# Optimization experiments

Hardware: AMD Instinct MI355X
Metric: run time of the kernel (lower is better)

Reference implementation:

```python
import jax, jax.numpy as jnp
import numpy as np

VOCAB = 45
MAX_LEN = 250
E = 1024
H = 8
F = 4096
L = 6
B = 32
S = 256


def layer_norm(x, g, b, eps=1e-5):
    m = x.mean(-1, keepdims=True)
    v = ((x - m) ** 2).mean(-1, keepdims=True)
    return (x - m) / jnp.sqrt(v + eps) * g + b


def setup_inputs() -> dict:
    key = jax.random.key(0)
    ks = jax.random.split(key, 20)
    s = 0.02
    inp = {
        "sequences": jax.random.randint(ks[0], (B, S), 1, VOCAB),  # avoid PAD id 0
        "token_emb": jax.random.normal(ks[1], (VOCAB, E), jnp.float32) * s,
        "dist_emb": jax.random.normal(ks[2], (MAX_LEN + 1, H), jnp.float32) * s,
        "Wqkv": jax.random.normal(ks[3], (L, 3 * E, E), jnp.float32) * s,
        "bqkv": jnp.zeros((L, 3 * E), jnp.float32),
        "Wo": jax.random.normal(ks[4], (L, E, E), jnp.float32) * s,
        "bo": jnp.zeros((L, E), jnp.float32),
        "W1": jax.random.normal(ks[5], (L, F, E), jnp.float32) * s,
        "b1": jnp.zeros((L, F), jnp.float32),
        "W2": jax.random.normal(ks[6], (L, E, F), jnp.float32) * s,
        "b2": jnp.zeros((L, E), jnp.float32),
        "ln1_g": jnp.ones((L, E), jnp.float32),
        "ln1_b": jnp.zeros((L, E), jnp.float32),
        "ln2_g": jnp.ones((L, E), jnp.float32),
        "ln2_b": jnp.zeros((L, E), jnp.float32),
        "fn_g": jnp.ones((E,), jnp.float32),
        "fn_b": jnp.zeros((E,), jnp.float32),
        "gen_W": jax.random.normal(ks[7], (VOCAB, E), jnp.float32) * s,
        "gen_b": jnp.zeros((VOCAB,), jnp.float32),
    }
    return inp


def reference(sequences, token_emb, dist_emb, Wqkv, bqkv, Wo, bo, W1, b1, W2, b2,
              ln1_g, ln1_b, ln2_g, ln2_b, fn_g, fn_b, gen_W, gen_b):
    Bsz, Slen = sequences.shape
    Emb = token_emb.shape[1]
    nH = dist_emb.shape[1]
    Dh = Emb // nH

    x = token_emb[sequences] * jnp.sqrt(jnp.float32(Emb))  # [B,S,E]

    idx = jnp.arange(Slen)
    dist = jnp.minimum(jnp.abs(idx[None, :] - idx[:, None]), dist_emb.shape[0] - 1)
    bias = jnp.transpose(dist_emb[dist], (2, 0, 1))  # [H,S,S]
    causal = idx[None, :] <= idx[:, None]  # key <= query (lower-triangular allowed)
    mask = jnp.where(causal[None, :, :], bias, jnp.float32(-1e9))  # [H,S,S]

    scale = 1.0 / jnp.sqrt(jnp.float32(Dh))
    nL = Wqkv.shape[0]
    for l in range(nL):
        qkv = x @ Wqkv[l].T + bqkv[l]  # [B,S,3E]
        q, k, v = jnp.split(qkv, 3, axis=-1)
        q = q.reshape(Bsz, Slen, nH, Dh)
        k = k.reshape(Bsz, Slen, nH, Dh)
        v = v.reshape(Bsz, Slen, nH, Dh)
        scores = jnp.einsum('bqhd,bkhd->bhqk', q, k) * scale + mask[None]
        attn = jax.nn.softmax(scores, axis=-1)
        o = jnp.einsum('bhqk,bkhd->bqhd', attn, v).reshape(Bsz, Slen, Emb)
        o = o @ Wo[l].T + bo[l]
        x = layer_norm(x + o, ln1_g[l], ln1_b[l])
        h = jax.nn.gelu(x @ W1[l].T + b1[l], approximate=False)
        h = h @ W2[l].T + b2[l]
        x = layer_norm(x + h, ln2_g[l], ln2_b[l])

    x = layer_norm(x, fn_g, fn_b)
    logits = x @ gen_W.T + gen_b  # [B,S,VOCAB]
    return logits
```

## Files before the change

kernel.cpp:

```cpp
#include <hip/hip_runtime.h>
#include <hip/hip_bf16.h>

typedef __hip_bfloat16 bf16;
typedef __attribute__((ext_vector_type(8))) short short8;
typedef __attribute__((ext_vector_type(4))) float f32x4;

#define GLB_AS(p) ((const __attribute__((address_space(1))) void*)(p))
#define LDS_AS(p) ((__attribute__((address_space(3))) void*)(p))

template<int EPI>
__global__ __launch_bounds__(512, 2) void gemm8p(
    const bf16* __restrict__ A, const bf16* __restrict__ Bm, bf16* __restrict__ C,
    int K, int lda, int ldb, int ldc, const float* __restrict__ bias)
{
    __shared__ __align__(16) bf16 Als[2][2][8192];
    __shared__ __align__(16) bf16 Bls[2][2][8192];

    const int tid  = threadIdx.x;
    const int wave = tid >> 6;
    const int lane = tid & 63;
    const int wr = wave >> 2;
    const int wc = wave & 3;

    const int Mt = gridDim.x, Nt = gridDim.y;
    int pid = blockIdx.y * Mt + blockIdx.x;
    const int cpx = (Mt * Nt) >> 3;
    pid = (pid & 7) * cpx + (pid >> 3);
    int m_t, n_t;
    {
        const int grpsz = 8 * Nt;
        const int grp = pid / grpsz;
        const int first = grp * 8;
        int rem = Mt - first; if (rem > 8) rem = 8;
        const int loc = pid - grp * grpsz;
        m_t = first + loc % rem;
        n_t = loc / rem;
    }
    const int m0 = m_t << 8;
    const int n0 = n_t << 8;
    const int nt = K >> 6;

    const int s_r  = tid >> 2;
    const int s_sl = ((tid & 3) ^ ((tid >> 3) & 3)) << 3;
    const bf16* As0 = A  + (long)(m0 + s_r) * lda + s_sl;
    const bf16* Bs0 = Bm + (long)(n0 + s_r) * ldb + s_sl;
    const long ldal = (long)lda << 7;
    const long ldbl = (long)ldb << 7;
    char* AB = (char*)Als;
    char* BB = (char*)Bls;
    const int wofs = wave << 10;

#define STAGE_A(d, kh, tt) do { \
    const bf16* g_ = As0 + ((long)(tt) << 6) + ((kh) << 5); \
    char* dst_ = AB + ((((d) << 1) + (kh)) << 14) + wofs; \
    __builtin_amdgcn_global_load_lds(GLB_AS(g_), LDS_AS(dst_), 16, 0, 0); \
    __builtin_amdgcn_global_load_lds(GLB_AS(g_ + ldal), LDS_AS(dst_ + 8192), 16, 0, 0); \
  } while (0)
#define STAGE_B(d, kh, tt) do { \
    const bf16* g_ = Bs0 + ((long)(tt) << 6) + ((kh) << 5); \
    char* dst_ = BB + ((((d) << 1) + (kh)) << 14) + wofs; \
    __builtin_amdgcn_global_load_lds(GLB_AS(g_), LDS_AS(dst_), 16, 0, 0); \
    __builtin_amdgcn_global_load_lds(GLB_AS(g_ + ldbl), LDS_AS(dst_ + 8192), 16, 0, 0); \
  } while (0)
#define BAR() do { asm volatile("" ::: "memory"); \
    __builtin_amdgcn_s_barrier(); asm volatile("" ::: "memory"); } while (0)

    STAGE_B(0, 0, 0); STAGE_A(0, 0, 0); STAGE_B(0, 1, 0); STAGE_A(0, 1, 0);
    STAGE_B(1, 0, 1); STAGE_A(1, 0, 1); STAGE_B(1, 1, 1);

    f32x4 acc[8][4];
#pragma unroll
    for (int i = 0; i < 8; ++i)
#pragma unroll
        for (int j = 0; j < 4; ++j) acc[i][j] = (f32x4){0.f, 0.f, 0.f, 0.f};

    const int fr  = lane & 15;
    const int swz = (((lane >> 4) ^ ((lane >> 1) & 3)) << 4);
    const int aoff = (wr << 13) + fr * 64 + swz;
    const int boff = (wc << 12) + fr * 64 + swz;

    asm volatile("s_waitcnt vmcnt(6)" ::: "memory");
    __builtin_amdgcn_s_barrier();
    asm volatile("" ::: "memory");

    int d = 0;
    for (int t = 0; t < nt; ++t, d ^= 1) {
        short8 b[4];
#pragma unroll
        for (int p = 0; p < 4; ++p) {
            const int kh = p >> 1, rh = p & 1;
            const char* Ahb = AB + (((d << 1) + kh) << 14);
            const char* Bhb = BB + (((d << 1) + kh) << 14);
            short8 a[4];
#pragma unroll
            for (int i = 0; i < 4; ++i)
                a[i] = *(const short8*)(Ahb + aoff + rh * 4096 + i * 1024);
            if ((p & 1) == 0) {
#pragma unroll
                for (int j = 0; j < 4; ++j)
                    b[j] = *(const short8*)(Bhb + boff + j * 1024);
            }
            if (p == 0)      { if (t + 1 < nt) STAGE_A(d ^ 1, 1, t + 1); }
            else if (p == 1) { if (t + 2 < nt) STAGE_B(d, 0, t + 2); }
            else if (p == 2) { if (t + 2 < nt) STAGE_A(d, 0, t + 2); }
            else             { if (t + 2 < nt) STAGE_B(d, 1, t + 2); }
            BAR();
            asm volatile("s_waitcnt lgkmcnt(0)" ::: "memory");
            __builtin_amdgcn_sched_barrier(0);
            __builtin_amdgcn_s_setprio(1);
#pragma unroll
            for (int i = 0; i < 4; ++i)
#pragma unroll
                for (int j = 0; j < 4; ++j)
                    acc[rh * 4 + i][j] = __builtin_amdgcn_mfma_f32_16x16x32_bf16(
                        a[i], b[j], acc[rh * 4 + i][j], 0, 0, 0);
            __builtin_amdgcn_s_setprio(0);
            if (p == 3 && t < nt - 1) {
                if (t == nt - 2) asm volatile("s_waitcnt vmcnt(0)" ::: "memory");
                else             asm volatile("s_waitcnt vmcnt(6)" ::: "memory");
            }
            BAR();
        }
    }
#undef STAGE_A
#undef STAGE_B
#undef BAR

    const int ccol = lane & 15;
    const int crow = (lane >> 4) << 2;
    const int colb  = n0 + (wc << 6) + ccol;
    const int rowbb = m0 + (wr << 7) + crow;
#pragma unroll
    for (int j = 0; j < 4; ++j) {
        const int col = colb + (j << 4);
        const float bv = bias[col];
#pragma unroll
        for (int i = 0; i < 8; ++i) {
            const int rowb = rowbb + (i << 4);
#pragma unroll
            for (int r2 = 0; r2 < 4; ++r2) {
                float v = acc[i][j][r2] + bv;
                if (EPI == 2) v = 0.5f * v * (1.0f + erff(v * 0.70710678118f));
                C[(long)(rowb + r2) * ldc + col] = __float2bfloat16(v);
            }
        }
    }
}

template<int EPI>
__global__ __launch_bounds__(256) void gemm_bf16(
    const bf16* __restrict__ Ain, const bf16* __restrict__ Bin, void* __restrict__ Cv,
    int K, int lda, int ldb, int ldc,
    long sAo, long sAi, long sBo, long sBi, long sCo, long sCi, int nInner,
    const float* __restrict__ bias, const float* __restrict__ demb,
    float scale)
{
    __shared__ __align__(16) bf16 Als[128 * 64];
    __shared__ __align__(16) bf16 Bls[128 * 64];

    const int z  = blockIdx.z;
    const int zo = z / nInner;
    const int zi = z - zo * nInner;
    const bf16* A = Ain + zo * sAo + zi * sAi;
    const bf16* B = Bin + zo * sBo + zi * sBi;
    const long coff = zo * sCo + zi * sCi;

    int m_t, n_t;
    if (EPI == 3) {
        m_t = (blockIdx.x + 1) >> 1;
        n_t = blockIdx.x >> 1;
    } else {
        const int Mt = gridDim.x, Nt = gridDim.y;
        if (Mt >= 8) {
            const int pid = blockIdx.y * Mt + blockIdx.x;
            const int grpsz = 8 * Nt;
            const int grp = pid / grpsz;
            const int first = grp * 8;
            int rem = Mt - first; if (rem > 8) rem = 8;
            const int loc = pid - grp * grpsz;
            m_t = first + loc % rem;
            n_t = loc / rem;
        } else { m_t = blockIdx.x; n_t = blockIdx.y; }
    }
    const int m0 = m_t * 128;
    const int n0 = n_t * 128;

    const int Keff = (EPI == 4) ? (m_t + 1) * 128 : K;

    const int tid  = threadIdx.x;
    const int wave = tid >> 6;
    const int lane = tid & 63;
    const int wm = (wave >> 1) * 64;
    const int wn = (wave & 1) * 64;

    f32x4 acc[4][4];
#pragma unroll
    for (int i = 0; i < 4; ++i)
#pragma unroll
        for (int j = 0; j < 4; ++j) acc[i][j] = (f32x4){0.f, 0.f, 0.f, 0.f};

    const int srow = lane >> 3;
    const int scol = (((lane & 7) ^ srow) << 3);

    for (int k0 = 0; k0 < Keff; k0 += 64) {
        __syncthreads();
#pragma unroll
        for (int c = 0; c < 4; ++c) {
            const int chunk = (wave << 2) + c;
            const int row = (chunk << 3) + srow;
            const bf16* ga = A + (long)(m0 + row) * lda + k0 + scol;
            const bf16* gb = B + (long)(n0 + row) * ldb + k0 + scol;
            __builtin_amdgcn_global_load_lds(GLB_AS(ga), LDS_AS(&Als[chunk << 9]), 16, 0, 0);
            __builtin_amdgcn_global_load_lds(GLB_AS(gb), LDS_AS(&Bls[chunk << 9]), 16, 0, 0);
        }
        __syncthreads();

#pragma unroll
        for (int kk = 0; kk < 2; ++kk) {
            const int CB = (kk << 2) + (lane >> 4);
            const int r = lane & 15;
            short8 afr[4], bfr[4];
#pragma unroll
            for (int i = 0; i < 4; ++i) {
                const int ar = wm + (i << 4) + r;
                afr[i] = *(const short8*)&Als[ar * 64 + ((CB ^ (ar & 7)) << 3)];
            }
#pragma unroll
            for (int j = 0; j < 4; ++j) {
                const int br = wn + (j << 4) + r;
                bfr[j] = *(const short8*)&Bls[br * 64 + ((CB ^ (br & 7)) << 3)];
            }
#pragma unroll
            for (int i = 0; i < 4; ++i)
#pragma unroll
                for (int j = 0; j < 4; ++j)
                    acc[i][j] = __builtin_amdgcn_mfma_f32_16x16x32_bf16(
                        afr[i], bfr[j], acc[i][j], 0, 0, 0);
        }
    }

    const int ccol = lane & 15;
    const int crow = (lane >> 4) << 2;
#pragma unroll
    for (int i = 0; i < 4; ++i) {
#pragma unroll
        for (int j = 0; j < 4; ++j) {
            const int col  = n0 + wn + (j << 4) + ccol;
            const int rowb = m0 + wm + (i << 4) + crow;
#pragma unroll
            for (int r2 = 0; r2 < 4; ++r2) {
                const int row = rowb + r2;
                float v = acc[i][j][r2];
                const long cidx = coff + (long)row * ldc + col;
                if (EPI == 3) {
                    int d0 = row - col;
                    int ad = d0 < 0 ? -d0 : d0;
                    if (ad > 250) ad = 250;
                    ((bf16*)Cv)[cidx] = __float2bfloat16(v * scale + demb[ad * 8 + zi]);
                } else if (EPI == 0) {
                    if (bias) v += bias[col];
                    ((float*)Cv)[cidx] = v;
                } else if (EPI == 1 || EPI == 4) {
                    if (bias) v += bias[col];
                    ((bf16*)Cv)[cidx] = __float2bfloat16(v);
                } else {
                    v += bias[col];
                    v = 0.5f * v * (1.0f + erff(v * 0.70710678118f));
                    ((bf16*)Cv)[cidx] = __float2bfloat16(v);
                }
            }
        }
    }
}

__global__ void cast4_kernel(const float* __restrict__ s0, const float* __restrict__ s1,
                             const float* __restrict__ s2, const float* __restrict__ s3,
                             bf16* __restrict__ d0, bf16* __restrict__ d1,
                             bf16* __restrict__ d2, bf16* __restrict__ d3,
                             long n0, long n1, long n2, long n3)
{
    long i = (long)blockIdx.x * blockDim.x + threadIdx.x;
    const float* s; bf16* d; long base;
    if (i < n0)                { s = s0; d = d0; base = 0; }
    else if (i < n0 + n1)      { s = s1; d = d1; base = n0; }
    else if (i < n0 + n1 + n2) { s = s2; d = d2; base = n0 + n1; }
    else if (i < n0+n1+n2+n3)  { s = s3; d = d3; base = n0 + n1 + n2; }
    else return;
    const long j = i - base;
    f32x4 v = *(const f32x4*)(s + j * 4);
    bf16 t[4] = {__float2bfloat16(v[0]), __float2bfloat16(v[1]),
                 __float2bfloat16(v[2]), __float2bfloat16(v[3])};
    *(short4*)(d + j * 4) = *(const short4*)t;
}

__global__ void embed_kernel(const int* __restrict__ seq, const float* __restrict__ emb,
                             float* __restrict__ x, bf16* __restrict__ xb)
{
    const long t = blockIdx.x;
    const int tok = seq[t];
    const int tid = threadIdx.x;
    f32x4 v = *(const f32x4*)(emb + (long)tok * 1024 + tid * 4);
    v *= 32.0f;
    *(f32x4*)(x + t * 1024 + tid * 4) = v;
    bf16 tq[4] = {__float2bfloat16(v[0]), __float2bfloat16(v[1]),
                  __float2bfloat16(v[2]), __float2bfloat16(v[3])};
    *(short4*)(xb + t * 1024 + tid * 4) = *(const short4*)tq;
}

__global__ void softmax_kernel(const bf16* __restrict__ scores, bf16* __restrict__ probs)
{
    const long row = (long)blockIdx.x * 4 + (threadIdx.x >> 6);
    const int q = (int)(row & 255);
    const int lane = threadIdx.x & 63;
    const int kbase = lane * 4;
    short4 sv = *(const short4*)(scores + row * 256 + kbase);
    const bf16* sp = (const bf16*)&sv;
    float v0 = (kbase + 0 <= q) ? __bfloat162float(sp[0]) : -1e30f;
    float v1 = (kbase + 1 <= q) ? __bfloat162float(sp[1]) : -1e30f;
    float v2 = (kbase + 2 <= q) ? __bfloat162float(sp[2]) : -1e30f;
    float v3 = (kbase + 3 <= q) ? __bfloat162float(sp[3]) : -1e30f;
    float m = fmaxf(fmaxf(v0, v1), fmaxf(v2, v3));
#pragma unroll
    for (int off = 32; off; off >>= 1) m = fmaxf(m, __shfl_xor(m, off));
    float e0 = (kbase + 0 <= q) ? __expf(v0 - m) : 0.f;
    float e1 = (kbase + 1 <= q) ? __expf(v1 - m) : 0.f;
    float e2 = (kbase + 2 <= q) ? __expf(v2 - m) : 0.f;
    float e3 = (kbase + 3 <= q) ? __expf(v3 - m) : 0.f;
    float s = e0 + e1 + e2 + e3;
#pragma unroll
    for (int off = 32; off; off >>= 1) s += __shfl_xor(s, off);
    const float inv = 1.0f / s;
    bf16 tq[4] = {__float2bfloat16(e0 * inv), __float2bfloat16(e1 * inv),
                  __float2bfloat16(e2 * inv), __float2bfloat16(e3 * inv)};
    *(short4*)(probs + row * 256 + kbase) = *(const short4*)tq;
}

__global__ void transpose_v(const bf16* __restrict__ qkv, bf16* __restrict__ vt)
{
    __shared__ bf16 tile[32][33];
    const int bh = blockIdx.y;
    const int st = blockIdx.x & 7;
    const int dt = blockIdx.x >> 3;
    const int tx = threadIdx.x & 31;
    const int ty = threadIdx.x >> 5;
    const int b = bh >> 3, h = bh & 7;
    const bf16* src = qkv + ((long)b * 256) * 3072 + 2048 + h * 128 + dt * 32;
#pragma unroll
    for (int i = 0; i < 4; ++i) {
        const int s = st * 32 + ty * 4 + i;
        tile[ty * 4 + i][tx] = src[(long)s * 3072 + tx];
    }
    __syncthreads();
    bf16* dst = vt + ((long)bh * 128 + dt * 32) * 256 + st * 32;
#pragma unroll
    for (int i = 0; i < 4; ++i) {
        const int dl = ty * 4 + i;
        dst[(long)dl * 256 + tx] = tile[tx][dl];
    }
}

__global__ void ln_kernel(const float* __restrict__ x, const bf16* __restrict__ res,
                          const float* __restrict__ g, const float* __restrict__ bta,
                          float* __restrict__ outf, bf16* __restrict__ outb,
                          int has_res, int has_bf)
{
    const long t = blockIdx.x;
    const int tid = threadIdx.x;
    f32x4 v = *(const f32x4*)(x + t * 1024 + tid * 4);
    if (has_res) {
        short4 rv = *(const short4*)(res + t * 1024 + tid * 4);
        const bf16* rp = (const bf16*)&rv;
#pragma unroll
        for (int q = 0; q < 4; ++q) v[q] += __bfloat162float(rp[q]);
    }
    float s  = v[0] + v[1] + v[2] + v[3];
    float ss = v[0]*v[0] + v[1]*v[1] + v[2]*v[2] + v[3]*v[3];
#pragma unroll
    for (int off = 32; off; off >>= 1) {
        s  += __shfl_xor(s, off);
        ss += __shfl_xor(ss, off);
    }
    __shared__ float red[8];
    const int w = tid >> 6;
    if ((tid & 63) == 0) { red[w] = s; red[4 + w] = ss; }
    __syncthreads();
    s  = red[0] + red[1] + red[2] + red[3];
    ss = red[4] + red[5] + red[6] + red[7];
    const float mean = s * (1.0f / 1024.0f);
    const float var  = ss * (1.0f / 1024.0f) - mean * mean;
    const float rstd = rsqrtf(var + 1e-5f);
    f32x4 gv = *(const f32x4*)(g + tid * 4);
    f32x4 bv = *(const f32x4*)(bta + tid * 4);
    f32x4 o;
#pragma unroll
    for (int q = 0; q < 4; ++q) o[q] = (v[q] - mean) * rstd * gv[q] + bv[q];
    *(f32x4*)(outf + t * 1024 + tid * 4) = o;
    if (has_bf) {
        bf16 tq[4] = {__float2bfloat16(o[0]), __float2bfloat16(o[1]),
                      __float2bfloat16(o[2]), __float2bfloat16(o[3])};
        *(short4*)(outb + t * 1024 + tid * 4) = *(const short4*)tq;
    }
}

__global__ void gen_kernel(const float* __restrict__ xf, const float* __restrict__ W,
                           const float* __restrict__ bias, float* __restrict__ out)
{
    const long t = (long)blockIdx.x * 4 + (threadIdx.x >> 6);
    const int lane = threadIdx.x & 63;
    const float* xr = xf + t * 1024;
    float xv[16];
#pragma unroll
    for (int j = 0; j < 16; ++j) xv[j] = xr[lane + 64 * j];
    for (int n = 0; n < 45; ++n) {
        const float* wr = W + (long)n * 1024;
        float a = 0.f;
#pragma unroll
        for (int j = 0; j < 16; ++j) a += xv[j] * wr[lane + 64 * j];
#pragma unroll
        for (int off = 32; off; off >>= 1) a += __shfl_xor(a, off);
        if (lane == 0) out[t * 45 + n] = a + bias[n];
    }
}

extern "C" void kernel_launch(void* const* d_in, const int* in_sizes, int n_in,
                              void* d_out, int out_size, void* d_ws, size_t ws_size,
                              hipStream_t stream)
{
    (void)in_sizes; (void)n_in; (void)out_size; (void)ws_size;
    const int*   seq  = (const int*)d_in[0];
    const float* temb = (const float*)d_in[1];
    const float* demb = (const float*)d_in[2];
    const float* Wqkv = (const float*)d_in[3];
    const float* bqkv = (const float*)d_in[4];
    const float* Wo   = (const float*)d_in[5];
    const float* bo   = (const float*)d_in[6];
    const float* W1   = (const float*)d_in[7];
    const float* b1   = (const float*)d_in[8];
    const float* W2   = (const float*)d_in[9];
    const float* b2   = (const float*)d_in[10];
    const float* ln1g = (const float*)d_in[11];
    const float* ln1b = (const float*)d_in[12];
    const float* ln2g = (const float*)d_in[13];
    const float* ln2b = (const float*)d_in[14];
    const float* fng  = (const float*)d_in[15];
    const float* fnb  = (const float*)d_in[16];
    const float* genW = (const float*)d_in[17];
    const float* genb = (const float*)d_in[18];
    float* out = (float*)d_out;

    char* ws = (char*)d_ws;
    size_t off = 0;
    auto alloc = [&](size_t bytes) -> char* {
        char* p = ws + off;
        off += (bytes + 255) & ~(size_t)255;
        return p;
    };

    bf16*  wqkv_l = (bf16*)alloc(3072ULL * 1024 * 2);
    bf16*  wo_l   = (bf16*)alloc(1024ULL * 1024 * 2);
    bf16*  w1_l   = (bf16*)alloc(4096ULL * 1024 * 2);
    bf16*  w2_l   = (bf16*)alloc(1024ULL * 4096 * 2);
    float* x      = (float*)alloc(8192ULL * 1024 * 4);
    bf16*  xb     = (bf16*)alloc(8192ULL * 1024 * 2);
    char*  qkvreg = alloc(8192ULL * 3072 * 2);
    char*  R      = alloc(8192ULL * 4096 * 2);
    bf16*  tmpb   = (bf16*)alloc(8192ULL * 1024 * 2);

    bf16*  qkvb   = (bf16*)qkvreg;
    bf16*  attnb  = (bf16*)qkvreg;
    float* lnout  = (float*)qkvreg;
    bf16*  scoreb = (bf16*)R;
    bf16*  probs  = (bf16*)(R + 8192ULL * 4096);
    bf16*  vt     = (bf16*)R;
    bf16*  hbuf   = (bf16*)R;

    const dim3 blk(256);
    const dim3 blk8(512);

    embed_kernel<<<8192, blk, 0, stream>>>(seq, temb, x, xb);

    for (int l = 0; l < 6; ++l) {
        cast4_kernel<<<12288, blk, 0, stream>>>(
            Wqkv + (long)l * 3072 * 1024, Wo + (long)l * 1024 * 1024,
            W1 + (long)l * 4096 * 1024,   W2 + (long)l * 4096 * 1024,
            wqkv_l, wo_l, w1_l, w2_l,
            786432, 262144, 1048576, 1048576);

        gemm8p<1><<<dim3(32, 12), blk8, 0, stream>>>(xb, wqkv_l, qkvb,
            1024, 1024, 1024, 3072, bqkv + (long)l * 3072);

        gemm_bf16<3><<<dim3(3, 1, 256), blk, 0, stream>>>(qkvb, qkvb + 1024, scoreb,
            128, 3072, 3072, 256,
            786432, 128, 786432, 128, 524288, 65536, 8,
            nullptr, demb, 0.08838834764831845f);

        softmax_kernel<<<16384, blk, 0, stream>>>(scoreb, probs);
        transpose_v<<<dim3(32, 256), blk, 0, stream>>>(qkvb, vt);

        gemm_bf16<4><<<dim3(2, 1, 256), blk, 0, stream>>>(probs, vt, attnb,
            256, 256, 256, 1024,
            524288, 65536, 262144, 32768, 262144, 128, 8,
            nullptr, nullptr, 0.f);

        gemm8p<1><<<dim3(32, 4), blk8, 0, stream>>>(attnb, wo_l, tmpb,
            1024, 1024, 1024, 1024, bo + (long)l * 1024);

        ln_kernel<<<8192, blk, 0, stream>>>(x, tmpb, ln1g + (long)l * 1024,
                                            ln1b + (long)l * 1024, x, xb, 1, 1);

        gemm8p<2><<<dim3(32, 16), blk8, 0, stream>>>(xb, w1_l, hbuf,
            1024, 1024, 1024, 4096, b1 + (long)l * 4096);

        gemm8p<1><<<dim3(32, 4), blk8, 0, stream>>>(hbuf, w2_l, tmpb,
            4096, 4096, 4096, 1024, b2 + (long)l * 1024);

        ln_kernel<<<8192, blk, 0, stream>>>(x, tmpb, ln2g + (long)l * 1024,
                                            ln2b + (long)l * 1024, x, xb, 1, 1);
    }

    ln_kernel<<<8192, blk, 0, stream>>>(x, nullptr, fng, fnb, lnout, nullptr, 0, 0);
    gen_kernel<<<2048, blk, 0, stream>>>(lnout, genW, genb, out);
}
```

Measured before the change: 3.016 ms.

## Route N=1024 GEMMs to 128x128 kernel and precompute addressing in gemm_bf16

The Wo and W2 projections (N=1024) now use the 128x128-tile gemm_bf16 kernel on a 64x8 grid instead of the 256x256 pipelined gemm8p, which only launched 128 blocks. The aim is better CU occupancy on these narrower GEMMs. gemm_bf16 now hoists global and LDS address arithmetic out of the k-loop and sets a 3-blocks-per-CU launch bound. gemm8p drops a sched_barrier and reorders its epilogue stores so each row is written contiguously. The tradeoff is that the simpler kernel has no multi-stage prefetch, so memory latency may be less well hidden on the K=4096 W2 GEMM.

Result: faster. 2.685 ms (-11.0%).

```diff
diff --git a/kernel.cpp b/kernel.cpp
--- a/kernel.cpp
+++ b/kernel.cpp
@@ -106,7 +106,6 @@
             else             { if (t + 2 < nt) STAGE_B(d, 1, t + 2); }
             BAR();
             asm volatile("s_waitcnt lgkmcnt(0)" ::: "memory");
-            __builtin_amdgcn_sched_barrier(0);
             __builtin_amdgcn_s_setprio(1);
 #pragma unroll
             for (int i = 0; i < 4; ++i)
@@ -130,25 +129,27 @@
     const int crow = (lane >> 4) << 2;
     const int colb  = n0 + (wc << 6) + ccol;
     const int rowbb = m0 + (wr << 7) + crow;
-#pragma unroll
-    for (int j = 0; j < 4; ++j) {
-        const int col = colb + (j << 4);
-        const float bv = bias[col];
-#pragma unroll
-        for (int i = 0; i < 8; ++i) {
-            const int rowb = rowbb + (i << 4);
-#pragma unroll
-            for (int r2 = 0; r2 < 4; ++r2) {
-                float v = acc[i][j][r2] + bv;
+    float bv[4];
+#pragma unroll
+    for (int j = 0; j < 4; ++j) bv[j] = bias[colb + (j << 4)];
+#pragma unroll
+    for (int i = 0; i < 8; ++i) {
+#pragma unroll
+        for (int r2 = 0; r2 < 4; ++r2) {
+            const int row = rowbb + (i << 4) + r2;
+            bf16* cp = C + (long)row * ldc + colb;
+#pragma unroll
+            for (int j = 0; j < 4; ++j) {
+                float v = acc[i][j][r2] + bv[j];
                 if (EPI == 2) v = 0.5f * v * (1.0f + erff(v * 0.70710678118f));
-                C[(long)(rowb + r2) * ldc + col] = __float2bfloat16(v);
+                cp[j << 4] = __float2bfloat16(v);
             }
         }
     }
 }
 
 template<int EPI>
-__global__ __launch_bounds__(256) void gemm_bf16(
+__global__ __launch_bounds__(256, 3) void gemm_bf16(
     const bf16* __restrict__ Ain, const bf16* __restrict__ Bin, void* __restrict__ Cv,
     int K, int lda, int ldb, int ldc,
     long sAo, long sAi, long sBo, long sBi, long sCo, long sCi, int nInner,
@@ -201,35 +202,57 @@
 
     const int srow = lane >> 3;
     const int scol = (((lane & 7) ^ srow) << 3);
+    const bf16* gaP[4];
+    const bf16* gbP[4];
+    bf16* ldsA[4];
+    bf16* ldsB[4];
+#pragma unroll
+    for (int c = 0; c < 4; ++c) {
+        const int chunk = (wave << 2) + c;
+        const int row = (chunk << 3) + srow;
+        gaP[c] = A + (long)(m0 + row) * lda + scol;
+        gbP[c] = B + (long)(n0 + row) * ldb + scol;
+        ldsA[c] = &Als[chunk << 9];
+        ldsB[c] = &Bls[chunk << 9];
+    }
+
+    const int r   = lane & 15;
+    const int cb0 = lane >> 4;
+    int aofs[2][4], bofs[2][4];
+#pragma unroll
+    for (int kk = 0; kk < 2; ++kk) {
+        const int CB = (kk << 2) + cb0;
+#pragma unroll
+        for (int i = 0; i < 4; ++i) {
+            const int ar = wm + (i << 4) + r;
+            aofs[kk][i] = ar * 128 + ((CB ^ (ar & 7)) << 4);
+            const int br = wn + (i << 4) + r;
+            bofs[kk][i] = br * 128 + ((CB ^ (br & 7)) << 4);
+        }
+    }
+    const char* AbB = (const char*)Als;
+    const char* BbB = (const char*)Bls;
 
     for (int k0 = 0; k0 < Keff; k0 += 64) {
         __syncthreads();
 #pragma unroll
         for (int c = 0; c < 4; ++c) {
-            const int chunk = (wave << 2) + c;
-            const int row = (chunk << 3) + srow;
-            const bf16* ga = A + (long)(m0 + row) * lda + k0 + scol;
-            const bf16* gb = B + (long)(n0 + row) * ldb + k0 + scol;
-            __builtin_amdgcn_global_load_lds(GLB_AS(ga), LDS_AS(&Als[chunk << 9]), 16, 0, 0);
-            __builtin_amdgcn_global_load_lds(GLB_AS(gb), LDS_AS(&Bls[chunk << 9]), 16, 0, 0);
+            __builtin_amdgcn_global_load_lds(GLB_AS(gaP[c]), LDS_AS(ldsA[c]), 16, 0, 0);
+            __builtin_amdgcn_global_load_lds(GLB_AS(gbP[c]), LDS_AS(ldsB[c]), 16, 0, 0);
+            gaP[c] += 64;
+            gbP[c] += 64;
         }
         __syncthreads();
 
 #pragma unroll
         for (int kk = 0; kk < 2; ++kk) {
-            const int CB = (kk << 2) + (lane >> 4);
-            const int r = lane & 15;
             short8 afr[4], bfr[4];
 #pragma unroll
-            for (int i = 0; i < 4; ++i) {
-                const int ar = wm + (i << 4) + r;
-                afr[i] = *(const short8*)&Als[ar * 64 + ((CB ^ (ar & 7)) << 3)];
-            }
-#pragma unroll
-            for (int j = 0; j < 4; ++j) {
-                const int br = wn + (j << 4) + r;
-                bfr[j] = *(const short8*)&Bls[br * 64 + ((CB ^ (br & 7)) << 3)];
-            }
+            for (int i = 0; i < 4; ++i)
+                afr[i] = *(const short8*)(AbB + aofs[kk][i]);
+#pragma unroll
+            for (int j = 0; j < 4; ++j)
+                bfr[j] = *(const short8*)(BbB + bofs[kk][j]);
 #pragma unroll
             for (int i = 0; i < 4; ++i)
 #pragma unroll
@@ -502,8 +525,9 @@
             524288, 65536, 262144, 32768, 262144, 128, 8,
             nullptr, nullptr, 0.f);
 
-        gemm8p<1><<<dim3(32, 4), blk8, 0, stream>>>(attnb, wo_l, tmpb,
-            1024, 1024, 1024, 1024, bo + (long)l * 1024);
+        gemm_bf16<1><<<dim3(64, 8, 1), blk, 0, stream>>>(attnb, wo_l, tmpb,
+            1024, 1024, 1024, 1024, 0, 0, 0, 0, 0, 0, 1,
+            bo + (long)l * 1024, nullptr, 0.f);
 
         ln_kernel<<<8192, blk, 0, stream>>>(x, tmpb, ln1g + (long)l * 1024,
                                             ln1b + (long)l * 1024, x, xb, 1, 1);
@@ -511,8 +535,9 @@
         gemm8p<2><<<dim3(32, 16), blk8, 0, stream>>>(xb, w1_l, hbuf,
             1024, 1024, 1024, 4096, b1 + (long)l * 4096);
 
-        gemm8p<1><<<dim3(32, 4), blk8, 0, stream>>>(hbuf, w2_l, tmpb,
-            4096, 4096, 4096, 1024, b2 + (long)l * 1024);
+        gemm_bf16<1><<<dim3(64, 8, 1), blk, 0, stream>>>(hbuf, w2_l, tmpb,
+            4096, 4096, 4096, 1024, 0, 0, 0, 0, 0, 0, 1,
+            b2 + (long)l * 1024, nullptr, 0.f);
 
         ln_kernel<<<8192, blk, 0, stream>>>(x, tmpb, ln2g + (long)l * 1024,
                                             ln2b + (long)l * 1024, x, xb, 1, 1);
```
